# Kernel tuning notes

Measured on AMD Instinct MI355X. Metric: run time of the kernel, lower is better.

## Reference

```python
import jax, jax.numpy as jnp
import numpy as np

N = 2560          # 64 graphs * 40 nodes (hard-coded by view(64,40,40))
E = 163840        # edges, avg degree 64
HEADS = 4
IN_C = 32
H0 = 128          # hidden_dims[0] per head
H1 = 128          # hidden_dims[1] per head
OUT_E = 40
EPS_BN = 1e-5


def _glorot(key, shape):
    fan = sum(shape[-2:]) if len(shape) > 1 else shape[0]
    return jax.random.normal(key, shape, dtype=jnp.float32) * (2.0 / fan) ** 0.5


def setup_inputs() -> dict:
    key = jax.random.key(0)
    ks = jax.random.split(key, 24)
    inp = {
        "x": jax.random.normal(ks[0], (N, IN_C), dtype=jnp.float32),
        "edge_index": jax.random.randint(ks[1], (2, E), 0, N, dtype=jnp.int32),
        "pos": jax.random.normal(ks[2], (N, 2), dtype=jnp.float32),
        "mask": jax.random.randint(ks[3], (N,), 0, 2, dtype=jnp.int32),
        "adjacency": jax.random.uniform(ks[4], (N, OUT_E), dtype=jnp.float32),
        # GAT layer 1 (in -> heads*H0)
        "W1": _glorot(ks[5], (IN_C, HEADS * H0)),
        "att_src1": _glorot(ks[6], (HEADS, H0)),
        "att_dst1": _glorot(ks[7], (HEADS, H0)),
        "We1": _glorot(ks[8], (1, HEADS * H0)),
        "att_e1": _glorot(ks[9], (HEADS, H0)),
        "bias1": jnp.zeros((HEADS * H0,), dtype=jnp.float32),
        # BatchNorm 1
        "g1": jnp.ones((HEADS * H0,), dtype=jnp.float32),
        "be1": jnp.zeros((HEADS * H0,), dtype=jnp.float32),
        # GAT layer 2 (heads*H0 -> heads*H1)
        "W2": _glorot(ks[10], (HEADS * H0, HEADS * H1)),
        "att_src2": _glorot(ks[11], (HEADS, H1)),
        "att_dst2": _glorot(ks[12], (HEADS, H1)),
        "We2": _glorot(ks[13], (1, HEADS * H1)),
        "att_e2": _glorot(ks[14], (HEADS, H1)),
        "bias2": jnp.zeros((HEADS * H1,), dtype=jnp.float32),
        # BatchNorm 2
        "g2": jnp.ones((HEADS * H1,), dtype=jnp.float32),
        "be2": jnp.zeros((HEADS * H1,), dtype=jnp.float32),
        # fc_edge
        "Wfc": _glorot(ks[15], (HEADS * H1, OUT_E)),
        "bfc": jnp.zeros((OUT_E,), dtype=jnp.float32),
    }
    return inp


def _gat(x, src, dst, ew, W, att_s, att_d, We, att_e, bias, heads, c):
    # x: [N, Fin] -> h: [N, H, C]
    h = (x @ W).reshape(-1, heads, c)
    a_s = (h * att_s).sum(-1)                       # [N, H]
    a_d = (h * att_d).sum(-1)                       # [N, H]
    he = (ew[:, None] @ We).reshape(-1, heads, c)   # [E, H, C] edge attr proj
    a_e = (he * att_e).sum(-1)                      # [E, H]
    alpha = jax.nn.leaky_relu(a_s[src] + a_d[dst] + a_e, 0.2)
    # segment softmax over destination nodes
    m = jax.ops.segment_max(alpha, dst, num_segments=N)
    alpha = jnp.exp(alpha - m[dst])
    denom = jax.ops.segment_sum(alpha, dst, num_segments=N)
    alpha = alpha / (denom[dst] + 1e-16)
    out = jax.ops.segment_sum(h[src] * alpha[:, :, None], dst, num_segments=N)
    return out.reshape(-1, heads * c) + bias


def _batchnorm(x, g, b):
    mu = x.mean(0)
    var = x.var(0)
    return (x - mu) * jax.lax.rsqrt(var + EPS_BN) * g + b


def reference(x, edge_index, pos, mask, adjacency,
              W1, att_src1, att_dst1, We1, att_e1, bias1, g1, be1,
              W2, att_src2, att_dst2, We2, att_e2, bias2, g2, be2,
              Wfc, bfc):
    src, dst = edge_index[0], edge_index[1]
    ew = 1.0 / (jnp.linalg.norm(pos[src] - pos[dst], axis=1) + 1e-6)  # [E]

    h = _gat(x, src, dst, ew, W1, att_src1, att_dst1, We1, att_e1, bias1, HEADS, H0)
    h = jax.nn.relu(_batchnorm(h, g1, be1))

    e = _gat(h, src, dst, ew, W2, att_src2, att_dst2, We2, att_e2, bias2, HEADS, H1)
    e = jax.nn.relu(_batchnorm(e, g2, be2))

    out_edge = e @ Wfc + bfc                     # [N, 40]
    out_edge = out_edge * mask[:, None].astype(out_edge.dtype)
    out_edge = out_edge.reshape(64, 40, 40)
    return out_edge + adjacency.reshape(64, 40, 40)
```

## Files before the change

kernel.cpp:

```cpp
#include <hip/hip_runtime.h>
#include <hip/hip_bf16.h>

#define NN 2560
#define NE 163840
#define NH 4
#define NC 128
#define NF 512
#define OUTE 40

typedef short bf16x8 __attribute__((ext_vector_type(8)));
typedef float f32x4 __attribute__((ext_vector_type(4)));

__device__ inline ushort f2bf(float f) {
    uint u = __float_as_uint(f);
    uint r = u + 0x7FFF + ((u >> 16) & 1);
    return (ushort)(r >> 16);
}
__device__ inline float bflo(uint v) { return __uint_as_float(v << 16); }
__device__ inline float bfhi(uint v) { return __uint_as_float(v & 0xFFFF0000u); }

__global__ void k_prep(const int* __restrict__ ei, int* __restrict__ deg,
                       int* __restrict__ rank,
                       const float* __restrict__ We1, const float* __restrict__ ae1,
                       const float* __restrict__ We2, const float* __restrict__ ae2,
                       float* __restrict__ dote,
                       const float* __restrict__ Wfc, ushort* __restrict__ WfcT,
                       const float* __restrict__ W2, ushort* __restrict__ W2T) {
    __shared__ ushort tile[64][72];
    int b = blockIdx.x;
    if (b < 640) {
        int e = b * 256 + threadIdx.x;
        rank[e] = atomicAdd(&deg[ei[NE + e]], 1);
    } else if (b < 642) {
        int t = threadIdx.x;
        const float* W = (b == 641) ? We2 : We1;
        const float* A = (b == 641) ? ae2 : ae1;
        int w = t >> 6, l = t & 63;
        float p = W[w * 128 + l] * A[w * 128 + l] + W[w * 128 + 64 + l] * A[w * 128 + 64 + l];
#pragma unroll
        for (int o = 32; o > 0; o >>= 1) p += __shfl_down(p, o);
        if (l == 0) dote[(b - 640) * 4 + w] = p;
    } else if (b < 738) {
        int idx = (b - 642) * 256 + threadIdx.x;
        int j = idx >> 9, k = idx & 511;
        WfcT[idx] = (j < OUTE) ? f2bf(Wfc[k * OUTE + j]) : (ushort)0;
    } else {
        int id = b - 738;
        int n0 = (id & 7) * 64, k0 = (id >> 3) * 64;
        int t = threadIdx.x;
        int r = t >> 2, cseg = (t & 3) * 16;
#pragma unroll
        for (int c = 0; c < 16; c += 4) {
            float4 v = *(const float4*)&W2[(k0 + r) * 512 + n0 + cseg + c];
            tile[cseg + c + 0][r] = f2bf(v.x);
            tile[cseg + c + 1][r] = f2bf(v.y);
            tile[cseg + c + 2][r] = f2bf(v.z);
            tile[cseg + c + 3][r] = f2bf(v.w);
        }
        __syncthreads();
        *(uint4*)&W2T[(n0 + r) * 512 + k0 + cseg]     = *(uint4*)&tile[r][cseg];
        *(uint4*)&W2T[(n0 + r) * 512 + k0 + cseg + 8] = *(uint4*)&tile[r][cseg + 8];
    }
}

__global__ void k_scan(const int* __restrict__ deg, int* __restrict__ offs) {
    __shared__ int cs[256];
    int t = threadIdx.x;
    int base = t * 10;
    int local[10];
    int s = 0;
#pragma unroll
    for (int i = 0; i < 10; i++) { local[i] = deg[base + i]; s += local[i]; }
    cs[t] = s;
    __syncthreads();
    for (int off = 1; off < 256; off <<= 1) {
        int v = (t >= off) ? cs[t - off] : 0;
        __syncthreads();
        cs[t] += v;
        __syncthreads();
    }
    int excl = (t == 0) ? 0 : cs[t - 1];
#pragma unroll
    for (int i = 0; i < 10; i++) { offs[base + i] = excl; excl += local[i]; }
    if (t == 255) offs[NN] = excl;
}

__global__ void k_csr_fill(const int* __restrict__ ei, const float* __restrict__ pos,
                           const int* __restrict__ offs, const int* __restrict__ rank,
                           int2* __restrict__ csrp) {
    int e = blockIdx.x * 256 + threadIdx.x;
    if (e >= NE) return;
    int s = ei[e], d = ei[NE + e];
    float dx = pos[2 * s] - pos[2 * d];
    float dy = pos[2 * s + 1] - pos[2 * d + 1];
    float w = 1.0f / (sqrtf(dx * dx + dy * dy) + 1e-6f);
    csrp[offs[d] + rank[e]] = make_int2(s, __float_as_int(w));
}

__global__ __launch_bounds__(256) void k_gemm1_att(const float* __restrict__ x,
        const float* __restrict__ W1, const float* __restrict__ atts,
        const float* __restrict__ attd, ushort* __restrict__ hb,
        float* __restrict__ as_, float* __restrict__ ad_) {
    __shared__ float s_x[4][32];
    __shared__ float4 s_red[4][4];
    int n0 = blockIdx.x * 4, t = threadIdx.x;
    if (t < 128) s_x[t >> 5][t & 31] = x[n0 * 32 + t];
    __syncthreads();
    float a0[4] = {0.f, 0.f, 0.f, 0.f}, a1[4] = {0.f, 0.f, 0.f, 0.f};
#pragma unroll
    for (int k = 0; k < 32; k++) {
        float w0 = W1[k * 512 + t];
        float w1 = W1[k * 512 + t + 256];
#pragma unroll
        for (int nn = 0; nn < 4; nn++) {
            a0[nn] += s_x[nn][k] * w0;
            a1[nn] += s_x[nn][k] * w1;
        }
    }
    float sa0 = atts[t], sa1 = atts[t + 256];
    float da0 = attd[t], da1 = attd[t + 256];
    int w = t >> 6, lane = t & 63;
#pragma unroll
    for (int nn = 0; nn < 4; nn++) {
        hb[(n0 + nn) * 512 + t] = f2bf(a0[nn]);
        hb[(n0 + nn) * 512 + t + 256] = f2bf(a1[nn]);
        float ps0 = a0[nn] * sa0, pd0 = a0[nn] * da0;
        float ps1 = a1[nn] * sa1, pd1 = a1[nn] * da1;
#pragma unroll
        for (int o = 32; o > 0; o >>= 1) {
            ps0 += __shfl_xor(ps0, o); pd0 += __shfl_xor(pd0, o);
            ps1 += __shfl_xor(ps1, o); pd1 += __shfl_xor(pd1, o);
        }
        if (lane == 0) s_red[w][nn] = make_float4(ps0, pd0, ps1, pd1);
    }
    __syncthreads();
    if (t < 4) {
        int nn = t, n = n0 + nn;
        float4 r0 = s_red[0][nn], r1 = s_red[1][nn], r2 = s_red[2][nn], r3 = s_red[3][nn];
        as_[n * 4 + 0] = r0.x + r1.x; as_[n * 4 + 1] = r2.x + r3.x;
        as_[n * 4 + 2] = r0.z + r1.z; as_[n * 4 + 3] = r2.z + r3.z;
        ad_[n * 4 + 0] = r0.y + r1.y; ad_[n * 4 + 1] = r2.y + r3.y;
        ad_[n * 4 + 2] = r0.w + r1.w; ad_[n * 4 + 3] = r2.w + r3.w;
    }
}

__global__ __launch_bounds__(256) void k_edge_agg(const int* __restrict__ offs,
        const int2* __restrict__ csrp, const float* __restrict__ as_,
        const float* __restrict__ ad_, const float* __restrict__ dote,
        const ushort* __restrict__ hb, const float* __restrict__ bias,
        float* __restrict__ out) {
    int w = threadIdx.x >> 6, lane = threadIdx.x & 63;
    int n = blockIdx.x * 2 + (w >> 1);
    int hp = w & 1;
    int h0 = 2 * hp;
    int beg = offs[n], deg = offs[n + 1] - beg;
    float ad0 = ad_[n * 4 + h0], ad1 = ad_[n * 4 + h0 + 1];
    float d0 = dote[h0], d1 = dote[h0 + 1];
    float La0 = -1e30f, La1 = -1e30f, Lb0 = -1e30f, Lb1 = -1e30f;
    int off0 = 0, off1 = 0;
    if (lane < deg) {
        int2 p = csrp[beg + lane];
        off0 = p.x * NF;
        float2 a = *(const float2*)&as_[p.x * 4 + h0];
        float ww = __int_as_float(p.y);
        float v0 = a.x + ad0 + ww * d0; La0 = v0 > 0.f ? v0 : 0.2f * v0;
        float v1 = a.y + ad1 + ww * d1; La1 = v1 > 0.f ? v1 : 0.2f * v1;
    }
    if (lane + 64 < deg) {
        int2 p = csrp[beg + lane + 64];
        off1 = p.x * NF;
        float2 a = *(const float2*)&as_[p.x * 4 + h0];
        float ww = __int_as_float(p.y);
        float v0 = a.x + ad0 + ww * d0; Lb0 = v0 > 0.f ? v0 : 0.2f * v0;
        float v1 = a.y + ad1 + ww * d1; Lb1 = v1 > 0.f ? v1 : 0.2f * v1;
    }
    float mx0 = fmaxf(La0, Lb0), mx1 = fmaxf(La1, Lb1);
    for (int e = 128 + lane; e < deg; e += 64) {
        int2 p = csrp[beg + e];
        float2 a = *(const float2*)&as_[p.x * 4 + h0];
        float ww = __int_as_float(p.y);
        float v0 = a.x + ad0 + ww * d0; v0 = v0 > 0.f ? v0 : 0.2f * v0;
        float v1 = a.y + ad1 + ww * d1; v1 = v1 > 0.f ? v1 : 0.2f * v1;
        mx0 = fmaxf(mx0, v0); mx1 = fmaxf(mx1, v1);
    }
#pragma unroll
    for (int o = 32; o > 0; o >>= 1) {
        mx0 = fmaxf(mx0, __shfl_xor(mx0, o));
        mx1 = fmaxf(mx1, __shfl_xor(mx1, o));
    }
    float Aa0 = __expf(La0 - mx0), Ab0 = __expf(Lb0 - mx0);
    float Aa1 = __expf(La1 - mx1), Ab1 = __expf(Lb1 - mx1);
    float s0 = Aa0 + Ab0, s1 = Aa1 + Ab1;
    for (int e = 128 + lane; e < deg; e += 64) {
        int2 p = csrp[beg + e];
        float2 a = *(const float2*)&as_[p.x * 4 + h0];
        float ww = __int_as_float(p.y);
        float v0 = a.x + ad0 + ww * d0; v0 = v0 > 0.f ? v0 : 0.2f * v0;
        float v1 = a.y + ad1 + ww * d1; v1 = v1 > 0.f ? v1 : 0.2f * v1;
        s0 += __expf(v0 - mx0); s1 += __expf(v1 - mx1);
    }
#pragma unroll
    for (int o = 32; o > 0; o >>= 1) {
        s0 += __shfl_xor(s0, o); s1 += __shfl_xor(s1, o);
    }
    float inv0 = 1.f / (s0 + 1e-16f), inv1 = 1.f / (s1 + 1e-16f);
    bool hi = lane >= 32;
    const ushort* hbase = hb + hp * 256 + 4 * lane;
    float4 acc = make_float4(0.f, 0.f, 0.f, 0.f);
    int m0 = min(deg, 64);
#pragma unroll 8
    for (int e = 0; e < m0; e++) {
        float al = __shfl(Aa0, e), ah = __shfl(Aa1, e);
        float a = hi ? ah : al;
        int o = __shfl(off0, e);
        uint2 v = *(const uint2*)(hbase + o);
        acc.x += a * bflo(v.x); acc.y += a * bfhi(v.x);
        acc.z += a * bflo(v.y); acc.w += a * bfhi(v.y);
    }
    int m1 = min(deg, 128);
#pragma unroll 8
    for (int e = 64; e < m1; e++) {
        float al = __shfl(Ab0, e - 64), ah = __shfl(Ab1, e - 64);
        float a = hi ? ah : al;
        int o = __shfl(off1, e - 64);
        uint2 v = *(const uint2*)(hbase + o);
        acc.x += a * bflo(v.x); acc.y += a * bfhi(v.x);
        acc.z += a * bflo(v.y); acc.w += a * bfhi(v.y);
    }
    for (int e = 128; e < deg; e++) {
        int2 p = csrp[beg + e];
        float2 aa = *(const float2*)&as_[p.x * 4 + h0];
        float ww = __int_as_float(p.y);
        float v0 = aa.x + ad0 + ww * d0; v0 = v0 > 0.f ? v0 : 0.2f * v0;
        float v1 = aa.y + ad1 + ww * d1; v1 = v1 > 0.f ? v1 : 0.2f * v1;
        float a = hi ? __expf(v1 - mx1) : __expf(v0 - mx0);
        uint2 v = *(const uint2*)(hbase + p.x * NF);
        acc.x += a * bflo(v.x); acc.y += a * bfhi(v.x);
        acc.z += a * bflo(v.y); acc.w += a * bfhi(v.y);
    }
    float inv = hi ? inv1 : inv0;
    int ch = hp * 256 + 4 * lane;
    float4 b4 = *(const float4*)&bias[ch];
    float4 o4 = make_float4(acc.x * inv + b4.x, acc.y * inv + b4.y,
                            acc.z * inv + b4.z, acc.w * inv + b4.w);
    *(float4*)&out[n * NF + ch] = o4;
}

__global__ void k_bnstats(const float* __restrict__ x, float* __restrict__ stats) {
    int t = threadIdx.x;
    int r0 = blockIdx.x * 64;
    float s = 0.f, s2 = 0.f;
    for (int r = r0; r < r0 + 64; r++) {
        float v = x[r * NF + t];
        s += v; s2 += v * v;
    }
    atomicAdd(&stats[t], s);
    atomicAdd(&stats[NF + t], s2);
}

__global__ __launch_bounds__(256) void k_gemm2_bn_att(const float* __restrict__ A,
        const float* __restrict__ stats, const float* __restrict__ g,
        const float* __restrict__ bb, const ushort* __restrict__ BT,
        const float* __restrict__ atts, const float* __restrict__ attd,
        ushort* __restrict__ Cb, float* __restrict__ as_, float* __restrict__ ad_) {
    __shared__ ushort As[128][40];
    __shared__ ushort Bs[128][40];
    __shared__ float s_scale[512], s_shift[512];
    __shared__ float s_ps[2][128], s_pd[2][128];
    int t = threadIdx.x;
    const float invn = 1.0f / (float)NN;
    {
        int j = t;
#pragma unroll
        for (int rep = 0; rep < 2; rep++, j += 256) {
            float mu = stats[j] * invn;
            float var = stats[NF + j] * invn - mu * mu;
            float sc = rsqrtf(var + 1e-5f) * g[j];
            s_scale[j] = sc;
            s_shift[j] = bb[j] - mu * sc;
        }
    }
    int head = blockIdx.x;
    int rowBase = blockIdx.y * 128, colBase = head * 128;
    int w = t >> 6, lane = t & 63;
    int wm = (w >> 1) * 64, wn = (w & 1) * 64;
    int lm = lane & 15, q = lane >> 4;
    f32x4 acc[4][4] = {};
    int sr = t >> 2, sk = (t & 3) * 8;
    for (int k0 = 0; k0 < 512; k0 += 32) {
        __syncthreads();
        int jb = k0 + sk;
        float sc[8], sh[8];
#pragma unroll
        for (int c = 0; c < 8; c++) { sc[c] = s_scale[jb + c]; sh[c] = s_shift[jb + c]; }
        const float* Ap0 = &A[(rowBase + sr) * 512 + jb];
        const float* Ap1 = Ap0 + 64 * 512;
        float4 a00 = *(const float4*)Ap0, a01 = *(const float4*)(Ap0 + 4);
        float4 a10 = *(const float4*)Ap1, a11 = *(const float4*)(Ap1 + 4);
        uint4 b0 = *(const uint4*)&BT[(colBase + sr) * 512 + jb];
        uint4 b1 = *(const uint4*)&BT[(colBase + 64 + sr) * 512 + jb];
        ushort pa0[8], pa1[8];
        const float* f0 = &a00.x; const float* f1 = &a10.x;
#pragma unroll
        for (int c = 0; c < 4; c++) {
            pa0[c] = f2bf(fmaxf(f0[c] * sc[c] + sh[c], 0.f));
            pa1[c] = f2bf(fmaxf(f1[c] * sc[c] + sh[c], 0.f));
        }
        const float* f2 = &a01.x; const float* f3 = &a11.x;
#pragma unroll
        for (int c = 0; c < 4; c++) {
            pa0[4 + c] = f2bf(fmaxf(f2[c] * sc[4 + c] + sh[4 + c], 0.f));
            pa1[4 + c] = f2bf(fmaxf(f3[c] * sc[4 + c] + sh[4 + c], 0.f));
        }
        *(uint4*)&As[sr][sk]      = *(uint4*)pa0;
        *(uint4*)&As[64 + sr][sk] = *(uint4*)pa1;
        *(uint4*)&Bs[sr][sk]      = b0;
        *(uint4*)&Bs[64 + sr][sk] = b1;
        __syncthreads();
        bf16x8 af[4], bf[4];
#pragma unroll
        for (int i = 0; i < 4; i++) af[i] = *(const bf16x8*)&As[wm + i * 16 + lm][q * 8];
#pragma unroll
        for (int j = 0; j < 4; j++) bf[j] = *(const bf16x8*)&Bs[wn + j * 16 + lm][q * 8];
#pragma unroll
        for (int i = 0; i < 4; i++)
#pragma unroll
            for (int j = 0; j < 4; j++)
                acc[i][j] = __builtin_amdgcn_mfma_f32_16x16x32_bf16(af[i], bf[j], acc[i][j], 0, 0, 0);
    }
#pragma unroll
    for (int i = 0; i < 4; i++) {
        int row = rowBase + wm + i * 16 + q * 4;
#pragma unroll
        for (int j = 0; j < 4; j++) {
            int col = colBase + wn + j * 16 + lm;
#pragma unroll
            for (int r = 0; r < 4; r++)
                Cb[(row + r) * 512 + col] = f2bf(acc[i][j][r]);
        }
    }
    float sa[4], da[4];
#pragma unroll
    for (int j = 0; j < 4; j++) {
        int col = colBase + wn + j * 16 + lm;
        sa[j] = atts[col]; da[j] = attd[col];
    }
#pragma unroll
    for (int i = 0; i < 4; i++) {
#pragma unroll
        for (int r = 0; r < 4; r++) {
            float ps = 0.f, pd = 0.f;
#pragma unroll
            for (int j = 0; j < 4; j++) {
                float c = acc[i][j][r];
                ps += c * sa[j]; pd += c * da[j];
            }
#pragma unroll
            for (int o = 1; o < 16; o <<= 1) { ps += __shfl_xor(ps, o); pd += __shfl_xor(pd, o); }
            if (lm == 0) {
                int row = wm + i * 16 + q * 4 + r;
                s_ps[w & 1][row] = ps; s_pd[w & 1][row] = pd;
            }
        }
    }
    __syncthreads();
    if (t < 128) {
        as_[(rowBase + t) * 4 + head] = s_ps[0][t] + s_ps[1][t];
    } else {
        int row = t - 128;
        ad_[(rowBase + row) * 4 + head] = s_pd[0][row] + s_pd[1][row];
    }
}

__global__ __launch_bounds__(64) void k_fc_bn(const float* __restrict__ e2,
        const float* __restrict__ stats, const float* __restrict__ g,
        const float* __restrict__ bb, const ushort* __restrict__ WfcT,
        const float* __restrict__ bfc, const int* __restrict__ mask,
        const float* __restrict__ adj, float* __restrict__ out) {
    __shared__ float s_scale[512], s_shift[512];
    int lane = threadIdx.x;
    const float invn = 1.0f / (float)NN;
    for (int j = lane; j < 512; j += 64) {
        float mu = stats[j] * invn;
        float var = stats[NF + j] * invn - mu * mu;
        float sc = rsqrtf(var + 1e-5f) * g[j];
        s_scale[j] = sc;
        s_shift[j] = bb[j] - mu * sc;
    }
    __syncthreads();
    int r0 = blockIdx.x * 16;
    int lm = lane & 15, q = lane >> 4;
    f32x4 acc[3] = {};
#pragma unroll
    for (int k0 = 0; k0 < 512; k0 += 32) {
        int jb = k0 + q * 8;
        const float* p = &e2[(r0 + lm) * 512 + jb];
        float4 v0 = *(const float4*)p, v1 = *(const float4*)(p + 4);
        ushort pa[8];
        const float* f0 = &v0.x; const float* f1 = &v1.x;
#pragma unroll
        for (int c = 0; c < 4; c++) {
            pa[c]     = f2bf(fmaxf(f0[c] * s_scale[jb + c] + s_shift[jb + c], 0.f));
            pa[4 + c] = f2bf(fmaxf(f1[c] * s_scale[jb + 4 + c] + s_shift[jb + 4 + c], 0.f));
        }
        bf16x8 af = *(const bf16x8*)pa;
#pragma unroll
        for (int jt = 0; jt < 3; jt++) {
            bf16x8 bf = *(const bf16x8*)&WfcT[(jt * 16 + lm) * 512 + k0 + q * 8];
            acc[jt] = __builtin_amdgcn_mfma_f32_16x16x32_bf16(af, bf, acc[jt], 0, 0, 0);
        }
    }
#pragma unroll
    for (int jt = 0; jt < 3; jt++) {
        int col = jt * 16 + lm;
        if (col < OUTE) {
#pragma unroll
            for (int r = 0; r < 4; r++) {
                int n = r0 + q * 4 + r;
                float v = acc[jt][r] + bfc[col];
                v = mask[n] ? v : 0.f;
                out[n * OUTE + col] = v + adj[n * OUTE + col];
            }
        }
    }
}

extern "C" void kernel_launch(void* const* d_in, const int* in_sizes, int n_in,
                              void* d_out, int out_size, void* d_ws, size_t ws_size,
                              hipStream_t stream) {
    const float* x       = (const float*)d_in[0];
    const int*   ei      = (const int*)d_in[1];
    const float* pos     = (const float*)d_in[2];
    const int*   mask    = (const int*)d_in[3];
    const float* adj     = (const float*)d_in[4];
    const float* W1      = (const float*)d_in[5];
    const float* atts1   = (const float*)d_in[6];
    const float* attd1   = (const float*)d_in[7];
    const float* We1     = (const float*)d_in[8];
    const float* atte1   = (const float*)d_in[9];
    const float* bias1   = (const float*)d_in[10];
    const float* g1      = (const float*)d_in[11];
    const float* be1     = (const float*)d_in[12];
    const float* W2      = (const float*)d_in[13];
    const float* atts2   = (const float*)d_in[14];
    const float* attd2   = (const float*)d_in[15];
    const float* We2     = (const float*)d_in[16];
    const float* atte2   = (const float*)d_in[17];
    const float* bias2   = (const float*)d_in[18];
    const float* g2      = (const float*)d_in[19];
    const float* be2     = (const float*)d_in[20];
    const float* Wfc     = (const float*)d_in[21];
    const float* bfc     = (const float*)d_in[22];
    float* out = (float*)d_out;

    char* ws = (char*)d_ws;
    int*    deg     = (int*)(ws);
    float*  stats   = (float*)(ws + 5120 * 4);
    int*    offs    = (int*)(ws + 7168 * 4);
    float*  dote    = (float*)(ws + 9744 * 4);
    int*    rank    = (int*)(ws + 9760 * 4);
    int2*   csrp    = (int2*)(ws + 173600 * 4);
    float*  as_     = (float*)(ws + 501280 * 4);
    float*  ad_     = (float*)(ws + 511520 * 4);
    float*  t1      = (float*)(ws + 521760 * 4);
    ushort* hb      = (ushort*)(ws + 1832480 * 4);
    ushort* W2T     = (ushort*)(ws + 2487840 * 4);
    ushort* WfcT    = (ushort*)(ws + 2618912 * 4);

    hipMemsetAsync(d_ws, 0, 7168 * 4, stream);

    k_prep<<<802, 256, 0, stream>>>(ei, deg, rank, We1, atte1, We2, atte2, dote,
                                    Wfc, WfcT, W2, W2T);
    k_scan<<<1, 256, 0, stream>>>(deg, offs);
    k_csr_fill<<<NE / 256, 256, 0, stream>>>(ei, pos, offs, rank, csrp);

    k_gemm1_att<<<NN / 4, 256, 0, stream>>>(x, W1, atts1, attd1, hb, as_, ad_);
    k_edge_agg<<<NN / 2, 256, 0, stream>>>(offs, csrp, as_, ad_, dote, hb, bias1, t1);
    k_bnstats<<<NN / 64, 512, 0, stream>>>(t1, stats);

    k_gemm2_bn_att<<<dim3(4, NN / 128), 256, 0, stream>>>(t1, stats, g1, be1, W2T,
                                                          atts2, attd2, hb, as_, ad_);
    k_edge_agg<<<NN / 2, 256, 0, stream>>>(offs, csrp, as_, ad_, dote + 4, hb, bias2, t1);
    k_bnstats<<<NN / 64, 512, 0, stream>>>(t1, stats + 1024);

    k_fc_bn<<<NN / 16, 64, 0, stream>>>(t1, stats + 1024, g2, be2, WfcT, bfc, mask, adj, out);
}
```

Measured before the change: 224.0 us.

## Replace CSR scan with fixed-stride adjacency slots plus overflow list, fuse fill into gemm1

After: 219.5 us. -2.0%, faster.

```diff
diff --git a/kernel.cpp b/kernel.cpp
--- a/kernel.cpp
+++ b/kernel.cpp
@@ -7,6 +7,7 @@
 #define NC 128
 #define NF 512
 #define OUTE 40
+#define CSTR 256
 
 typedef short bf16x8 __attribute__((ext_vector_type(8)));
 typedef float f32x4 __attribute__((ext_vector_type(4)));
@@ -63,47 +64,31 @@
     }
 }
 
-__global__ void k_scan(const int* __restrict__ deg, int* __restrict__ offs) {
-    __shared__ int cs[256];
-    int t = threadIdx.x;
-    int base = t * 10;
-    int local[10];
-    int s = 0;
-#pragma unroll
-    for (int i = 0; i < 10; i++) { local[i] = deg[base + i]; s += local[i]; }
-    cs[t] = s;
-    __syncthreads();
-    for (int off = 1; off < 256; off <<= 1) {
-        int v = (t >= off) ? cs[t - off] : 0;
-        __syncthreads();
-        cs[t] += v;
-        __syncthreads();
-    }
-    int excl = (t == 0) ? 0 : cs[t - 1];
-#pragma unroll
-    for (int i = 0; i < 10; i++) { offs[base + i] = excl; excl += local[i]; }
-    if (t == 255) offs[NN] = excl;
-}
-
-__global__ void k_csr_fill(const int* __restrict__ ei, const float* __restrict__ pos,
-                           const int* __restrict__ offs, const int* __restrict__ rank,
-                           int2* __restrict__ csrp) {
-    int e = blockIdx.x * 256 + threadIdx.x;
-    if (e >= NE) return;
-    int s = ei[e], d = ei[NE + e];
-    float dx = pos[2 * s] - pos[2 * d];
-    float dy = pos[2 * s + 1] - pos[2 * d + 1];
-    float w = 1.0f / (sqrtf(dx * dx + dy * dy) + 1e-6f);
-    csrp[offs[d] + rank[e]] = make_int2(s, __float_as_int(w));
-}
-
-__global__ __launch_bounds__(256) void k_gemm1_att(const float* __restrict__ x,
-        const float* __restrict__ W1, const float* __restrict__ atts,
-        const float* __restrict__ attd, ushort* __restrict__ hb,
-        float* __restrict__ as_, float* __restrict__ ad_) {
+__global__ __launch_bounds__(256) void k_csr_gemm1(const int* __restrict__ ei,
+        const float* __restrict__ pos, const int* __restrict__ rank,
+        int2* __restrict__ csrp, int* __restrict__ ovf_cnt, int4* __restrict__ ovf,
+        const float* __restrict__ x, const float* __restrict__ W1,
+        const float* __restrict__ atts, const float* __restrict__ attd,
+        ushort* __restrict__ hb, float* __restrict__ as_, float* __restrict__ ad_) {
     __shared__ float s_x[4][32];
     __shared__ float4 s_red[4][4];
-    int n0 = blockIdx.x * 4, t = threadIdx.x;
+    int b = blockIdx.x;
+    if (b < 640) {
+        int e = b * 256 + threadIdx.x;
+        int s = ei[e], d = ei[NE + e];
+        float dx = pos[2 * s] - pos[2 * d];
+        float dy = pos[2 * s + 1] - pos[2 * d + 1];
+        float w = 1.0f / (sqrtf(dx * dx + dy * dy) + 1e-6f);
+        int r = rank[e];
+        if (r < CSTR) {
+            csrp[(d << 8) + r] = make_int2(s, __float_as_int(w));
+        } else {
+            int i = atomicAdd(ovf_cnt, 1);
+            ovf[i] = make_int4(d, s, __float_as_int(w), 0);
+        }
+        return;
+    }
+    int n0 = (b - 640) * 4, t = threadIdx.x;
     if (t < 128) s_x[t >> 5][t & 31] = x[n0 * 32 + t];
     __syncthreads();
     float a0[4] = {0.f, 0.f, 0.f, 0.f}, a1[4] = {0.f, 0.f, 0.f, 0.f};
@@ -144,8 +129,9 @@
     }
 }
 
-__global__ __launch_bounds__(256) void k_edge_agg(const int* __restrict__ offs,
-        const int2* __restrict__ csrp, const float* __restrict__ as_,
+__global__ __launch_bounds__(256) void k_edge_agg(const int* __restrict__ deg_,
+        const int2* __restrict__ csrp, const int* __restrict__ ovf_cnt,
+        const int4* __restrict__ ovf, const float* __restrict__ as_,
         const float* __restrict__ ad_, const float* __restrict__ dote,
         const ushort* __restrict__ hb, const float* __restrict__ bias,
         float* __restrict__ out) {
@@ -153,12 +139,14 @@
     int n = blockIdx.x * 2 + (w >> 1);
     int hp = w & 1;
     int h0 = 2 * hp;
-    int beg = offs[n], deg = offs[n + 1] - beg;
+    int beg = n << 8;
+    int degn = deg_[n];
+    int dmain = min(degn, CSTR);
     float ad0 = ad_[n * 4 + h0], ad1 = ad_[n * 4 + h0 + 1];
     float d0 = dote[h0], d1 = dote[h0 + 1];
     float La0 = -1e30f, La1 = -1e30f, Lb0 = -1e30f, Lb1 = -1e30f;
     int off0 = 0, off1 = 0;
-    if (lane < deg) {
+    if (lane < dmain) {
         int2 p = csrp[beg + lane];
         off0 = p.x * NF;
         float2 a = *(const float2*)&as_[p.x * 4 + h0];
@@ -166,7 +154,7 @@
         float v0 = a.x + ad0 + ww * d0; La0 = v0 > 0.f ? v0 : 0.2f * v0;
         float v1 = a.y + ad1 + ww * d1; La1 = v1 > 0.f ? v1 : 0.2f * v1;
     }
-    if (lane + 64 < deg) {
+    if (lane + 64 < dmain) {
         int2 p = csrp[beg + lane + 64];
         off1 = p.x * NF;
         float2 a = *(const float2*)&as_[p.x * 4 + h0];
@@ -175,7 +163,7 @@
         float v1 = a.y + ad1 + ww * d1; Lb1 = v1 > 0.f ? v1 : 0.2f * v1;
     }
     float mx0 = fmaxf(La0, Lb0), mx1 = fmaxf(La1, Lb1);
-    for (int e = 128 + lane; e < deg; e += 64) {
+    for (int e = 128 + lane; e < dmain; e += 64) {
         int2 p = csrp[beg + e];
         float2 a = *(const float2*)&as_[p.x * 4 + h0];
         float ww = __int_as_float(p.y);
@@ -183,6 +171,19 @@
         float v1 = a.y + ad1 + ww * d1; v1 = v1 > 0.f ? v1 : 0.2f * v1;
         mx0 = fmaxf(mx0, v0); mx1 = fmaxf(mx1, v1);
     }
+    if (degn > CSTR) {
+        int oc = *ovf_cnt;
+        for (int i = lane; i < oc; i += 64) {
+            int4 o = ovf[i];
+            if (o.x == n) {
+                float2 a = *(const float2*)&as_[o.y * 4 + h0];
+                float ww = __int_as_float(o.z);
+                float v0 = a.x + ad0 + ww * d0; v0 = v0 > 0.f ? v0 : 0.2f * v0;
+                float v1 = a.y + ad1 + ww * d1; v1 = v1 > 0.f ? v1 : 0.2f * v1;
+                mx0 = fmaxf(mx0, v0); mx1 = fmaxf(mx1, v1);
+            }
+        }
+    }
 #pragma unroll
     for (int o = 32; o > 0; o >>= 1) {
         mx0 = fmaxf(mx0, __shfl_xor(mx0, o));
@@ -191,7 +192,7 @@
     float Aa0 = __expf(La0 - mx0), Ab0 = __expf(Lb0 - mx0);
     float Aa1 = __expf(La1 - mx1), Ab1 = __expf(Lb1 - mx1);
     float s0 = Aa0 + Ab0, s1 = Aa1 + Ab1;
-    for (int e = 128 + lane; e < deg; e += 64) {
+    for (int e = 128 + lane; e < dmain; e += 64) {
         int2 p = csrp[beg + e];
         float2 a = *(const float2*)&as_[p.x * 4 + h0];
         float ww = __int_as_float(p.y);
@@ -199,6 +200,19 @@
         float v1 = a.y + ad1 + ww * d1; v1 = v1 > 0.f ? v1 : 0.2f * v1;
         s0 += __expf(v0 - mx0); s1 += __expf(v1 - mx1);
     }
+    if (degn > CSTR) {
+        int oc = *ovf_cnt;
+        for (int i = lane; i < oc; i += 64) {
+            int4 o = ovf[i];
+            if (o.x == n) {
+                float2 a = *(const float2*)&as_[o.y * 4 + h0];
+                float ww = __int_as_float(o.z);
+                float v0 = a.x + ad0 + ww * d0; v0 = v0 > 0.f ? v0 : 0.2f * v0;
+                float v1 = a.y + ad1 + ww * d1; v1 = v1 > 0.f ? v1 : 0.2f * v1;
+                s0 += __expf(v0 - mx0); s1 += __expf(v1 - mx1);
+            }
+        }
+    }
 #pragma unroll
     for (int o = 32; o > 0; o >>= 1) {
         s0 += __shfl_xor(s0, o); s1 += __shfl_xor(s1, o);
@@ -207,8 +221,8 @@
     bool hi = lane >= 32;
     const ushort* hbase = hb + hp * 256 + 4 * lane;
     float4 acc = make_float4(0.f, 0.f, 0.f, 0.f);
-    int m0 = min(deg, 64);
-#pragma unroll 8
+    int m0 = min(dmain, 64);
+#pragma unroll 16
     for (int e = 0; e < m0; e++) {
         float al = __shfl(Aa0, e), ah = __shfl(Aa1, e);
         float a = hi ? ah : al;
@@ -217,7 +231,7 @@
         acc.x += a * bflo(v.x); acc.y += a * bfhi(v.x);
         acc.z += a * bflo(v.y); acc.w += a * bfhi(v.y);
     }
-    int m1 = min(deg, 128);
+    int m1 = min(dmain, 128);
 #pragma unroll 8
     for (int e = 64; e < m1; e++) {
         float al = __shfl(Ab0, e - 64), ah = __shfl(Ab1, e - 64);
@@ -227,7 +241,7 @@
         acc.x += a * bflo(v.x); acc.y += a * bfhi(v.x);
         acc.z += a * bflo(v.y); acc.w += a * bfhi(v.y);
     }
-    for (int e = 128; e < deg; e++) {
+    for (int e = 128; e < dmain; e++) {
         int2 p = csrp[beg + e];
         float2 aa = *(const float2*)&as_[p.x * 4 + h0];
         float ww = __int_as_float(p.y);
@@ -238,6 +252,22 @@
         acc.x += a * bflo(v.x); acc.y += a * bfhi(v.x);
         acc.z += a * bflo(v.y); acc.w += a * bfhi(v.y);
     }
+    if (degn > CSTR) {
+        int oc = *ovf_cnt;
+        for (int i = 0; i < oc; i++) {
+            int4 o = ovf[i];
+            if (o.x == n) {
+                float2 aa = *(const float2*)&as_[o.y * 4 + h0];
+                float ww = __int_as_float(o.z);
+                float v0 = aa.x + ad0 + ww * d0; v0 = v0 > 0.f ? v0 : 0.2f * v0;
+                float v1 = aa.y + ad1 + ww * d1; v1 = v1 > 0.f ? v1 : 0.2f * v1;
+                float a = hi ? __expf(v1 - mx1) : __expf(v0 - mx0);
+                uint2 v = *(const uint2*)(hbase + o.y * NF);
+                acc.x += a * bflo(v.x); acc.y += a * bfhi(v.x);
+                acc.z += a * bflo(v.y); acc.w += a * bfhi(v.y);
+            }
+        }
+    }
     float inv = hi ? inv1 : inv0;
     int ch = hp * 256 + 4 * lane;
     float4 b4 = *(const float4*)&bias[ch];
@@ -248,9 +278,9 @@
 
 __global__ void k_bnstats(const float* __restrict__ x, float* __restrict__ stats) {
     int t = threadIdx.x;
-    int r0 = blockIdx.x * 64;
+    int r0 = blockIdx.x * 32;
     float s = 0.f, s2 = 0.f;
-    for (int r = r0; r < r0 + 64; r++) {
+    for (int r = r0; r < r0 + 32; r++) {
         float v = x[r * NF + t];
         s += v; s2 += v * v;
     }
@@ -455,33 +485,35 @@
 
     char* ws = (char*)d_ws;
     int*    deg     = (int*)(ws);
+    int*    ovf_cnt = (int*)(ws + 2560 * 4);
     float*  stats   = (float*)(ws + 5120 * 4);
-    int*    offs    = (int*)(ws + 7168 * 4);
-    float*  dote    = (float*)(ws + 9744 * 4);
-    int*    rank    = (int*)(ws + 9760 * 4);
-    int2*   csrp    = (int2*)(ws + 173600 * 4);
-    float*  as_     = (float*)(ws + 501280 * 4);
-    float*  ad_     = (float*)(ws + 511520 * 4);
-    float*  t1      = (float*)(ws + 521760 * 4);
-    ushort* hb      = (ushort*)(ws + 1832480 * 4);
-    ushort* W2T     = (ushort*)(ws + 2487840 * 4);
-    ushort* WfcT    = (ushort*)(ws + 2618912 * 4);
+    float*  dote    = (float*)(ws + 7168 * 4);
+    int*    rank    = (int*)(ws + 7184 * 4);
+    int2*   csrp    = (int2*)(ws + 171024 * 4);
+    int4*   ovf     = (int4*)(ws + 1481744 * 4);
+    float*  as_     = (float*)(ws + 2137104 * 4);
+    float*  ad_     = (float*)(ws + 2147344 * 4);
+    float*  t1      = (float*)(ws + 2157584 * 4);
+    ushort* hb      = (ushort*)(ws + 3468304 * 4);
+    ushort* W2T     = (ushort*)(ws + 4123664 * 4);
+    ushort* WfcT    = (ushort*)(ws + 4254736 * 4);
 
     hipMemsetAsync(d_ws, 0, 7168 * 4, stream);
 
     k_prep<<<802, 256, 0, stream>>>(ei, deg, rank, We1, atte1, We2, atte2, dote,
                                     Wfc, WfcT, W2, W2T);
-    k_scan<<<1, 256, 0, stream>>>(deg, offs);
-    k_csr_fill<<<NE / 256, 256, 0, stream>>>(ei, pos, offs, rank, csrp);
-
-    k_gemm1_att<<<NN / 4, 256, 0, stream>>>(x, W1, atts1, attd1, hb, as_, ad_);
-    k_edge_agg<<<NN / 2, 256, 0, stream>>>(offs, csrp, as_, ad_, dote, hb, bias1, t1);
-    k_bnstats<<<NN / 64, 512, 0, stream>>>(t1, stats);
+    k_csr_gemm1<<<640 + NN / 4, 256, 0, stream>>>(ei, pos, rank, csrp, ovf_cnt, ovf,
+                                                  x, W1, atts1, attd1, hb, as_, ad_);
+
+    k_edge_agg<<<NN / 2, 256, 0, stream>>>(deg, csrp, ovf_cnt, ovf, as_, ad_,
+                                           dote, hb, bias1, t1);
+    k_bnstats<<<NN / 32, 512, 0, stream>>>(t1, stats);
 
     k_gemm2_bn_att<<<dim3(4, NN / 128), 256, 0, stream>>>(t1, stats, g1, be1, W2T,
                                                           atts2, attd2, hb, as_, ad_);
-    k_edge_agg<<<NN / 2, 256, 0, stream>>>(offs, csrp, as_, ad_, dote + 4, hb, bias2, t1);
-    k_bnstats<<<NN / 64, 512, 0, stream>>>(t1, stats + 1024);
+    k_edge_agg<<<NN / 2, 256, 0, stream>>>(deg, csrp, ovf_cnt, ovf, as_, ad_,
+                                           dote + 4, hb, bias2, t1);
+    k_bnstats<<<NN / 32, 512, 0, stream>>>(t1, stats + 1024);
 
     k_fc_bn<<<NN / 16, 64, 0, stream>>>(t1, stats + 1024, g2, be2, WfcT, bfc, mask, adj, out);
 }
```
